# Kernel tuning notes

Measured on AMD Instinct MI355X. Metric: run time of the kernel, lower is better.

Reference implementation:

```python
import jax, jax.numpy as jnp
import numpy as np


def conv2d(x, w, b):
    # NCHW input, OIHW kernel, SAME padding, stride 1
    y = jax.lax.conv_general_dilated(x, w, (1, 1), 'SAME',
                                     dimension_numbers=('NCHW', 'OIHW', 'NCHW'))
    return y + b[None, :, None, None]


def maxpool2(x):
    return jax.lax.reduce_window(x, -jnp.inf, jax.lax.max,
                                 (1, 1, 2, 2), (1, 1, 2, 2), 'VALID')


def gelu(x):
    return jax.nn.gelu(x, approximate=False)  # torch default exact GELU


def up2(x):
    # nearest-neighbor upsample x2 (torch Upsample mode='nearest')
    return jnp.repeat(jnp.repeat(x, 2, axis=2), 2, axis=3)


DIM = 32
CODEBOOK_SIZE = 512
COMMIT_W = 1.0


def setup_inputs() -> dict:
    key = jax.random.key(0)
    ks = jax.random.split(key, 10)
    s = 0.1
    return {
        'x': jax.random.normal(ks[0], (32, 1, 256, 256), jnp.float32),
        'e1_w': jax.random.normal(ks[1], (16, 1, 3, 3), jnp.float32) * s,
        'e1_b': jnp.zeros((16,), jnp.float32),
        'e2_w': jax.random.normal(ks[2], (32, 16, 3, 3), jnp.float32) * s,
        'e2_b': jnp.zeros((32,), jnp.float32),
        'codebook': jax.random.normal(ks[3], (CODEBOOK_SIZE, DIM), jnp.float32),
        'd1_w': jax.random.normal(ks[4], (16, 32, 3, 3), jnp.float32) * s,
        'd1_b': jnp.zeros((16,), jnp.float32),
        'd2_w': jax.random.normal(ks[5], (1, 16, 3, 3), jnp.float32) * s,
        'd2_b': jnp.zeros((1,), jnp.float32),
    }


def reference(x, e1_w, e1_b, e2_w, e2_b, codebook, d1_w, d1_b, d2_w, d2_b):
    # ---- encoder ----
    h = conv2d(x, e1_w, e1_b)
    h = maxpool2(h)
    h = gelu(h)
    h = conv2d(h, e2_w, e2_b)
    h = maxpool2(h)                      # [B, 32, H/4, W/4]

    # ---- vector quantize (accept_image_fmap=True) ----
    B, C, H, W = h.shape
    flat = h.transpose(0, 2, 3, 1).reshape(-1, C)          # [N, C] tokens
    # squared euclidean distances to codebook
    d = ((flat * flat).sum(-1, keepdims=True)
         - 2.0 * flat @ codebook.T
         + (codebook * codebook).sum(-1))                   # [N, K]
    idx = jnp.argmin(d, axis=-1)                            # [N] int
    q = codebook[idx]                                       # gather [N, C]
    commit_loss = COMMIT_W * jnp.mean((jax.lax.stop_gradient(q) - flat) ** 2)
    # straight-through estimator
    q = flat + jax.lax.stop_gradient(q - flat)
    hq = q.reshape(B, H, W, C).transpose(0, 3, 1, 2)        # back to NCHW
    indices = idx.reshape(B, H, W)

    # ---- decoder ----
    y = up2(hq)
    y = conv2d(y, d1_w, d1_b)
    y = gelu(y)
    y = up2(y)
    y = conv2d(y, d2_w, d2_b)
    return jnp.clip(y, -1.0, 1.0), indices, commit_loss
```

## Files before the change

### kernel.cpp

```cpp
#include <hip/hip_runtime.h>
#include <math.h>

#define GELU(v) (0.5f * (v) * (1.0f + erff((v)*0.70710678118654752440f)))

typedef __attribute__((ext_vector_type(8))) short short8;
typedef __attribute__((ext_vector_type(4))) float f32x4;
typedef __attribute__((ext_vector_type(16))) float f32x16;
#define MFMA16 __builtin_amdgcn_mfma_f32_16x16x32_bf16
#define MFMA32 __builtin_amdgcn_mfma_f32_32x32x16_bf16

#define SPLIT3(V, U1, U2, U3)                                                  \
  unsigned U1 = __float_as_uint(V) & 0xFFFF0000u;                              \
  float _r1 = (V)-__uint_as_float(U1);                                         \
  unsigned U2 = __float_as_uint(_r1) & 0xFFFF0000u;                            \
  float _r2 = _r1 - __uint_as_float(U2);                                       \
  unsigned U3 = __float_as_uint(_r2) & 0xFFFF0000u;

__global__ __launch_bounds__(256) void k_fold(const float* __restrict__ e2w,
                                              const float* __restrict__ d1w,
                                              const float* __restrict__ d2w,
                                              const float* __restrict__ cb,
                                              float* __restrict__ fwd2,
                                              unsigned short* __restrict__ cbs,
                                              float* __restrict__ csqg,
                                              unsigned short* __restrict__ wfrag,
                                              unsigned short* __restrict__ wfd1) {
  int i = blockIdx.x * 256 + threadIdx.x;
  if (i < 256) {
    int j = i;
    int pt = j & 15, ic = j >> 4;
    int a = pt >> 3, b2 = (pt >> 2) & 1, dy = (pt >> 1) & 1, dx = pt & 1;
    const float* wsrc = d2w + ic * 9;
    float s = 0.f;
    for (int ky = 0; ky < 3; ++ky) {
      int rm = (a == 0) ? (ky == 0 ? 0 : 1) : (ky == 2 ? 1 : 0);
      if (rm != dy) continue;
      for (int kx = 0; kx < 3; ++kx) {
        int cm = (b2 == 0) ? (kx == 0 ? 0 : 1) : (kx == 2 ? 1 : 0);
        if (cm == dx) s += wsrc[ky * 3 + kx];
      }
    }
    fwd2[j] = s;
  } else if (i < 16640) {
    int j = i - 256;
    float v = cb[j];
    SPLIT3(v, u1, u2, u3)
    cbs[j] = (unsigned short)(u1 >> 16);
    cbs[16384 + j] = (unsigned short)(u2 >> 16);
    cbs[32768 + j] = (unsigned short)(u3 >> 16);
  } else if (i < 17152) {
    int c = i - 16640;
    const float* row = cb + (size_t)c * 32;
    float s = 0.f;
#pragma unroll
    for (int d = 0; d < 32; ++d) s = fmaf(row[d], row[d], s);
    csqg[c] = s;
  } else if (i < 30976) {
    int j = i - 17152;
    int p = j / 4608, rem = j - p * 4608;
    int t = rem >> 9, l2 = (rem >> 3) & 63, jj = rem & 7;
    float v = e2w[((l2 & 31) * 16 + ((l2 >> 5) * 8 + jj)) * 9 + t];
    SPLIT3(v, u1, u2, u3)
    unsigned short r = (p == 0)   ? (unsigned short)(u1 >> 16)
                       : (p == 1) ? (unsigned short)(u2 >> 16)
                                  : (unsigned short)(u3 >> 16);
    wfrag[j] = r;
  } else if (i < 86272) {
    int j = i - 30976;
    int slot = j >> 9, l2 = (j >> 3) & 63, jj = j & 7;
    int cx = slot / 36, rem = slot % 36;
    int r3 = rem / 12, rem2 = rem % 12;
    int kh = rem2 / 6, rem3 = rem2 % 6;
    int pp = rem3 / 3, part = rem3 % 3;
    int c = l2 & 31, hi = l2 >> 5;
    int oc = c & 15, b2 = c >> 4;
    int ic = kh * 16 + hi * 8 + jj;
    int dy = r3 - pp, dx = cx - b2;
    float s = 0.f;
    if ((unsigned)dy < 2u && (unsigned)dx < 2u) {
      const float* wsrc = d1w + (oc * 32 + ic) * 9;
      for (int ky = 0; ky < 3; ++ky) {
        int rm = (pp == 0) ? (ky == 0 ? 0 : 1) : (ky == 2 ? 1 : 0);
        if (rm != dy) continue;
        for (int kx = 0; kx < 3; ++kx) {
          int cm = (b2 == 0) ? (kx == 0 ? 0 : 1) : (kx == 2 ? 1 : 0);
          if (cm == dx) s += wsrc[ky * 3 + kx];
        }
      }
    }
    SPLIT3(s, u1, u2, u3)
    unsigned short r = (part == 0)   ? (unsigned short)(u1 >> 16)
                       : (part == 1) ? (unsigned short)(u2 >> 16)
                                     : (unsigned short)(u3 >> 16);
    wfd1[j] = r;
  }
}

__global__ __launch_bounds__(256) void k_enc1(const float* __restrict__ x,
                                              const float* __restrict__ w,
                                              const float* __restrict__ bias,
                                              float* __restrict__ h1) {
  int n = blockIdx.x;
  int ysl = n & 7, m = n >> 3;
  int b = m & 31, k = m >> 5;
  int yy = ysl * 16 + k * 2 + (threadIdx.x >> 7);
  int xx = threadIdx.x & 127;
  const float* xp = x + (size_t)b * 65536;
  int r0 = 2 * yy - 1, c0 = 2 * xx - 1;
  float in[4][4];
#pragma unroll
  for (int i = 0; i < 4; ++i) {
    int r = r0 + i;
    bool rv = (unsigned)r < 256u;
#pragma unroll
    for (int j = 0; j < 4; ++j) {
      int c = c0 + j;
      in[i][j] = (rv && (unsigned)c < 256u) ? xp[r * 256 + c] : 0.0f;
    }
  }
  float vout[16];
#pragma unroll
  for (int oc = 0; oc < 16; ++oc) {
    const float* wp = w + oc * 9;
    float s00 = 0.f, s01 = 0.f, s10 = 0.f, s11 = 0.f;
#pragma unroll
    for (int ky = 0; ky < 3; ++ky)
#pragma unroll
      for (int kx = 0; kx < 3; ++kx) {
        float wv = wp[ky * 3 + kx];
        s00 = fmaf(in[ky][kx], wv, s00);
        s01 = fmaf(in[ky][kx + 1], wv, s01);
        s10 = fmaf(in[ky + 1][kx], wv, s10);
        s11 = fmaf(in[ky + 1][kx + 1], wv, s11);
      }
    float mm = fmaxf(fmaxf(s00, s01), fmaxf(s10, s11)) + bias[oc];
    vout[oc] = GELU(mm);
  }
  float* op = h1 + (size_t)b * 262144 + ((size_t)yy * 128 + xx) * 16;
#pragma unroll
  for (int q = 0; q < 4; ++q) {
    float4 vq;
    vq.x = vout[4 * q + 0]; vq.y = vout[4 * q + 1];
    vq.z = vout[4 * q + 2]; vq.w = vout[4 * q + 3];
    *(float4*)(op + 4 * q) = vq;
  }
}

__global__ __launch_bounds__(256) void k_enc2(const float* __restrict__ h1,
                                              const unsigned short* __restrict__ wfrag,
                                              const float* __restrict__ bias,
                                              float* __restrict__ h2) {
  __shared__ __align__(16) unsigned short sA[3 * 2 * 10 * 34 * 8];
  const int PP = 2 * 10 * 34 * 8;
  int tid = threadIdx.x;
  int n = blockIdx.x;
  int xcd = n & 7, m = n >> 3;
  int ty = xcd * 2 + (m & 1);
  int q0 = m >> 1;
  int b = q0 >> 2, xt = q0 & 3;
  int X0 = xt * 32, Y0 = ty * 8;
  const float* ip = h1 + (size_t)b * 262144;
  for (int g = tid; g < 680; g += 256) {
    int pos = g >> 1, ich = g & 1;
    int yy = pos / 34, xx = pos - yy * 34;
    int y = Y0 - 1 + yy, xg = X0 - 1 + xx;
    float4 v0 = {0.f, 0.f, 0.f, 0.f}, v1 = {0.f, 0.f, 0.f, 0.f};
    if ((unsigned)y < 128u && (unsigned)xg < 128u) {
      const float* sp = ip + ((size_t)y * 128 + xg) * 16 + ich * 8;
      v0 = *(const float4*)(sp);
      v1 = *(const float4*)(sp + 4);
    }
    float vv[8] = {v0.x, v0.y, v0.z, v0.w, v1.x, v1.y, v1.z, v1.w};
    short8 p1, p2, p3;
#pragma unroll
    for (int e = 0; e < 8; ++e) {
      SPLIT3(vv[e], u1, u2, u3)
      p1[e] = (short)(u1 >> 16);
      p2[e] = (short)(u2 >> 16);
      p3[e] = (short)(u3 >> 16);
    }
    int si = ((ich * 10 + yy) * 34 + xx) * 8;
    *(short8*)(sA + si) = p1;
    *(short8*)(sA + PP + si) = p2;
    *(short8*)(sA + 2 * PP + si) = p3;
  }
  __syncthreads();

  int l = tid & 63, w = tid >> 6;
  int xl = l & 31, ich = l >> 5;
  f32x16 acc0[2], acc1[2];
#pragma unroll
  for (int s = 0; s < 2; ++s)
#pragma unroll
    for (int r = 0; r < 16; ++r) { acc0[s][r] = 0.f; acc1[s][r] = 0.f; }

#pragma unroll
  for (int t = 0; t < 9; ++t) {
    int dy = t / 3, dx = t % 3;
    int s = t & 1;
    const unsigned short* wb = wfrag + t * 512 + l * 8;
    short8 bf1 = *(const short8*)(wb);
    short8 bf2 = *(const short8*)(wb + 4608);
    short8 bf3 = *(const short8*)(wb + 9216);
    int g0 = ((ich * 10) + (2 * w + dy)) * 34 + xl + dx;
    const unsigned short* a0p = sA + g0 * 8;
    short8 a01 = *(const short8*)(a0p);
    short8 a02 = *(const short8*)(a0p + PP);
    short8 a03 = *(const short8*)(a0p + 2 * PP);
    const unsigned short* a1p = a0p + 34 * 8;
    short8 a11 = *(const short8*)(a1p);
    short8 a12 = *(const short8*)(a1p + PP);
    short8 a13 = *(const short8*)(a1p + 2 * PP);
    acc0[s] = MFMA32(a01, bf1, acc0[s], 0, 0, 0);
    acc0[s] = MFMA32(a01, bf2, acc0[s], 0, 0, 0);
    acc0[s] = MFMA32(a02, bf1, acc0[s], 0, 0, 0);
    acc0[s] = MFMA32(a02, bf2, acc0[s], 0, 0, 0);
    acc0[s] = MFMA32(a01, bf3, acc0[s], 0, 0, 0);
    acc0[s] = MFMA32(a03, bf1, acc0[s], 0, 0, 0);
    acc1[s] = MFMA32(a11, bf1, acc1[s], 0, 0, 0);
    acc1[s] = MFMA32(a11, bf2, acc1[s], 0, 0, 0);
    acc1[s] = MFMA32(a12, bf1, acc1[s], 0, 0, 0);
    acc1[s] = MFMA32(a12, bf2, acc1[s], 0, 0, 0);
    acc1[s] = MFMA32(a11, bf3, acc1[s], 0, 0, 0);
    acc1[s] = MFMA32(a13, bf1, acc1[s], 0, 0, 0);
  }

  float bv = bias[l & 31];
  int ypool = (Y0 >> 1) + w;
  float* op = h2 + (size_t)b * 131072 + (size_t)(l & 31) * 4096 + ypool * 64 + (X0 >> 1);
#pragma unroll
  for (int k = 0; k < 8; ++k) {
    float e0 = (acc0[0][2 * k] + acc0[1][2 * k]);
    float o0 = (acc0[0][2 * k + 1] + acc0[1][2 * k + 1]);
    float e1 = (acc1[0][2 * k] + acc1[1][2 * k]);
    float o1 = (acc1[0][2 * k + 1] + acc1[1][2 * k + 1]);
    float mm = fmaxf(fmaxf(e0, o0), fmaxf(e1, o1)) + bv;
    int row = ((2 * k) & 3) + 8 * ((2 * k) >> 2) + 4 * ich;
    op[row >> 1] = mm;
  }
}

__global__ __launch_bounds__(256) void k_vq(const float* __restrict__ h2,
                                            const unsigned short* __restrict__ cbs,
                                            const float* __restrict__ csqg,
                                            float* __restrict__ idxout,
                                            float* __restrict__ partial) {
  __shared__ __align__(16) unsigned short sA[3 * 256 * 40];
  __shared__ float sFsq[256];
  __shared__ float sBd[256];
  __shared__ int sBi[256];
  __shared__ float sred[4];
  int tid = threadIdx.x;
  int blk = blockIdx.x;
  int t0 = blk * 256;
  size_t abase = (size_t)(t0 >> 12) * 131072 + (t0 & 4095);

  {
    const float* src = h2 + abase + tid;
    float fsq = 0.f;
#pragma unroll
    for (int g = 0; g < 4; ++g) {
      short8 p1, p2, p3;
#pragma unroll
      for (int e = 0; e < 8; ++e) {
        float v = src[(g * 8 + e) * 4096];
        fsq = fmaf(v, v, fsq);
        SPLIT3(v, u1, u2, u3)
        p1[e] = (short)(u1 >> 16);
        p2[e] = (short)(u2 >> 16);
        p3[e] = (short)(u3 >> 16);
      }
      *(short8*)(sA + (0 * 256 + tid) * 40 + g * 8) = p1;
      *(short8*)(sA + (1 * 256 + tid) * 40 + g * 8) = p2;
      *(short8*)(sA + (2 * 256 + tid) * 40 + g * 8) = p3;
    }
    sFsq[tid] = fsq;
  }
  __syncthreads();

  int l = tid & 63, w = tid >> 6;
  int cl = l & 15, k0 = (l >> 4) * 8;
  short8 af[3][4];
#pragma unroll
  for (int p = 0; p < 3; ++p)
#pragma unroll
    for (int tq = 0; tq < 4; ++tq) {
      int tok = w * 64 + tq * 16 + cl;
      af[p][tq] = *(const short8*)(sA + (p * 256 + tok) * 40 + k0);
    }

  float bd[4][4];
  int bi[4][4];
#pragma unroll
  for (int a = 0; a < 4; ++a)
#pragma unroll
    for (int b = 0; b < 4; ++b) { bd[a][b] = 3.4e38f; bi[a][b] = 0; }

#define LOADB(S, CT)                                                           \
  {                                                                            \
    int col = (CT)*16 + cl;                                                    \
    b1##S = *(const short8*)(cbs + (0 * 512 + col) * 32 + k0);                 \
    b2##S = *(const short8*)(cbs + (1 * 512 + col) * 32 + k0);                 \
    b3##S = *(const short8*)(cbs + (2 * 512 + col) * 32 + k0);                 \
    cq##S = csqg[col];                                                         \
  }
#define COMPUTE(S, CT)                                                         \
  {                                                                            \
    _Pragma("unroll") for (int tq = 0; tq < 4; ++tq) {                         \
      f32x4 acc = {0.f, 0.f, 0.f, 0.f};                                        \
      acc = MFMA16(af[0][tq], b1##S, acc, 0, 0, 0);                            \
      acc = MFMA16(af[0][tq], b2##S, acc, 0, 0, 0);                            \
      acc = MFMA16(af[1][tq], b1##S, acc, 0, 0, 0);                            \
      acc = MFMA16(af[1][tq], b2##S, acc, 0, 0, 0);                            \
      acc = MFMA16(af[0][tq], b3##S, acc, 0, 0, 0);                            \
      acc = MFMA16(af[2][tq], b1##S, acc, 0, 0, 0);                            \
      _Pragma("unroll") for (int i = 0; i < 4; ++i) {                          \
        float d = fmaf(-2.f, acc[i], cq##S);                                   \
        if (d < bd[tq][i]) { bd[tq][i] = d; bi[tq][i] = (CT)*16 + cl; }        \
      }                                                                        \
    }                                                                          \
  }

  short8 b1A, b2A, b3A, b1B, b2B, b3B;
  float cqA, cqB;
  LOADB(A, 0)
  LOADB(B, 1)
#pragma unroll 1
  for (int ct = 0; ct < 32; ct += 2) {
    COMPUTE(A, ct)
    LOADB(A, (ct + 2) & 31)
    COMPUTE(B, ct + 1)
    LOADB(B, (ct + 3) & 31)
  }
#undef LOADB
#undef COMPUTE

#pragma unroll
  for (int tq = 0; tq < 4; ++tq)
#pragma unroll
    for (int i = 0; i < 4; ++i)
#pragma unroll
      for (int m = 1; m < 16; m <<= 1) {
        float od = __shfl_xor(bd[tq][i], m, 64);
        int ob = __shfl_xor(bi[tq][i], m, 64);
        if (od < bd[tq][i] || (od == bd[tq][i] && ob < bi[tq][i])) {
          bd[tq][i] = od;
          bi[tq][i] = ob;
        }
      }
  if (cl == 0) {
#pragma unroll
    for (int tq = 0; tq < 4; ++tq)
#pragma unroll
      for (int i = 0; i < 4; ++i) {
        int tokl = w * 64 + tq * 16 + (l >> 4) * 4 + i;
        sBi[tokl] = bi[tq][i];
        sBd[tokl] = bd[tq][i];
      }
  }
  __syncthreads();

  idxout[t0 + tid] = (float)sBi[tid];
  float loss = sBd[tid] + sFsq[tid];
#pragma unroll
  for (int off = 32; off > 0; off >>= 1) loss += __shfl_down(loss, off, 64);
  if (l == 0) sred[w] = loss;
  __syncthreads();
  if (tid == 0) partial[blk] = (sred[0] + sred[1]) + (sred[2] + sred[3]);
}

__global__ __launch_bounds__(256) void k_loss(const float* __restrict__ partial,
                                              float* __restrict__ lossout) {
  __shared__ float sred[4];
  int tid = threadIdx.x;
  float v = partial[tid] + partial[tid + 256];
#pragma unroll
  for (int off = 32; off > 0; off >>= 1) v += __shfl_down(v, off, 64);
  if ((tid & 63) == 0) sred[tid >> 6] = v;
  __syncthreads();
  if (tid == 0)
    lossout[0] = ((sred[0] + sred[1]) + (sred[2] + sred[3])) * (1.0f / 4194304.0f);
}

__global__ __launch_bounds__(256, 2) void k_dec1(const float* __restrict__ idxf,
                                                 const unsigned short* __restrict__ cbs,
                                                 const unsigned short* __restrict__ wfd1,
                                                 const float* __restrict__ bias,
                                                 float* __restrict__ o) {
  __shared__ __align__(16) unsigned short sA[3 * 12240];
  __shared__ int sIdx[340];
  const int PP = 12240;
  int tid = threadIdx.x;
  int b = blockIdx.y;
  int qx0 = (blockIdx.x & 1) * 32, qy0 = (blockIdx.x >> 1) * 8;
  const float* ib = idxf + (size_t)b * 4096;
  for (int i = tid; i < 340; i += 256) {
    int yy = i / 34, xx = i % 34;
    int y = qy0 - 1 + yy, x = qx0 - 1 + xx;
    sIdx[i] = ((unsigned)y < 64u && (unsigned)x < 64u) ? (int)ib[y * 64 + x] : -1;
  }
  __syncthreads();
  for (int i = tid; i < 4080; i += 256) {
    int pos = i / 12, sub = i % 12, part = sub >> 2, g = sub & 3;
    int idx = sIdx[pos];
    short8 v = {0, 0, 0, 0, 0, 0, 0, 0};
    if (idx >= 0) v = *(const short8*)(cbs + ((part << 9) + idx) * 32 + g * 8);
    *(short8*)(sA + part * PP + pos * 36 + g * 8) = v;
  }
  __syncthreads();

  int l = tid & 63, w = tid >> 6;
  int xl = l & 31, hi = l >> 5;
  f32x16 acc[2][2];
#pragma unroll
  for (int s = 0; s < 2; ++s)
#pragma unroll
    for (int p2 = 0; p2 < 2; ++p2)
#pragma unroll
      for (int r = 0; r < 16; ++r) acc[s][p2][r] = 0.f;

#pragma unroll
  for (int cx = 0; cx < 3; ++cx) {
    short8 Bf[4][2][3];
#pragma unroll
    for (int q = 0; q < 4; ++q) {
      int r3 = (q == 0) ? 0 : (q == 3) ? 2 : 1;
      int pq = (q >= 2) ? 1 : 0;
#pragma unroll
      for (int kh = 0; kh < 2; ++kh)
#pragma unroll
        for (int pt = 0; pt < 3; ++pt) {
          int slot = cx * 36 + r3 * 12 + kh * 6 + pq * 3 + pt;
          Bf[q][kh][pt] = *(const short8*)(wfd1 + (size_t)slot * 512 + l * 8);
        }
    }
#pragma unroll
    for (int ar = 0; ar < 4; ++ar) {
#pragma unroll
      for (int kh = 0; kh < 2; ++kh) {
        const unsigned short* ap =
            sA + ((2 * w + ar) * 34 + xl + cx) * 36 + kh * 16 + hi * 8;
        short8 a1 = *(const short8*)(ap);
        short8 a2 = *(const short8*)(ap + PP);
        short8 a3 = *(const short8*)(ap + 2 * PP);
#pragma unroll
        for (int s = 0; s < 2; ++s) {
          int ry = ar - s;
          if (ry < 0 || ry > 2) continue;
#pragma unroll
          for (int p2 = 0; p2 < 2; ++p2) {
            if ((ry == 0 && p2 == 1) || (ry == 2 && p2 == 0)) continue;
            int q = ry + p2;
            f32x16 t = acc[s][p2];
            t = MFMA32(a1, Bf[q][kh][0], t, 0, 0, 0);
            t = MFMA32(a1, Bf[q][kh][1], t, 0, 0, 0);
            t = MFMA32(a2, Bf[q][kh][0], t, 0, 0, 0);
            t = MFMA32(a2, Bf[q][kh][1], t, 0, 0, 0);
            t = MFMA32(a1, Bf[q][kh][2], t, 0, 0, 0);
            t = MFMA32(a3, Bf[q][kh][0], t, 0, 0, 0);
            acc[s][p2] = t;
          }
        }
      }
    }
  }

  float bv = bias[l & 15];
  int b2 = (l >> 4) & 1;
  float* ob = o + (size_t)b * 262144 + (size_t)(l & 15) * 16384 + (qx0 << 1) + b2;
#pragma unroll
  for (int s = 0; s < 2; ++s) {
    int qy = qy0 + 2 * w + s;
#pragma unroll
    for (int p2 = 0; p2 < 2; ++p2) {
      int Y = 2 * qy + p2;
      float* op = ob + Y * 128;
#pragma unroll
      for (int reg = 0; reg < 16; ++reg) {
        int rowval = (reg & 3) + 8 * (reg >> 2) + 4 * hi;
        op[2 * rowval] = GELU(acc[s][p2][reg] + bv);
      }
    }
  }
}

__global__ __launch_bounds__(256) void k_dec2(const float* __restrict__ d1,
                                              const float* __restrict__ fwd2,
                                              const float* __restrict__ bias,
                                              float* __restrict__ out) {
  __shared__ float st[16 * 360];
  int tid = threadIdx.x;
  int b = blockIdx.y;
  int R0 = (blockIdx.x >> 3) * 16, C0 = (blockIdx.x & 7) * 16;
  const float* ip = d1 + (size_t)b * 262144;
  for (int i = tid; i < 5184; i += 256) {
    int ic = i / 324, rr = (i % 324) / 18, cc = i % 18;
    int r = R0 - 1 + rr, c = C0 - 1 + cc;
    st[ic * 360 + rr * 20 + cc] =
        ((unsigned)r < 128u && (unsigned)c < 128u) ? ip[ic * 16384 + r * 128 + c] : 0.f;
  }
  __syncthreads();
  int lane = tid & 63, wid = tid >> 6;
  int qy = wid >> 1, qx = wid & 1;
  int ty = qy * 8 + (lane >> 3), tx = qx * 8 + (lane & 7);
  float acc[4] = {0.f, 0.f, 0.f, 0.f};
#pragma unroll 1
  for (int ic = 0; ic < 16; ++ic) {
    const float* t = st + ic * 360 + ty * 20 + tx;
    float i3[3][3];
#pragma unroll
    for (int dy = 0; dy < 3; ++dy)
#pragma unroll
      for (int dx = 0; dx < 3; ++dx) i3[dy][dx] = t[dy * 20 + dx];
    const float* wp = fwd2 + ic * 16;
#pragma unroll
    for (int p = 0; p < 4; ++p) {
      int a = p >> 1, b2 = p & 1;
#pragma unroll
      for (int tp = 0; tp < 4; ++tp) {
        int dy = tp >> 1, dx = tp & 1;
        acc[p] = fmaf(i3[a + dy][b2 + dx], wp[p * 4 + tp], acc[p]);
      }
    }
  }
  float bv = bias[0];
  int Y = 2 * (R0 + ty), X = 2 * (C0 + tx);
  float* op = out + (size_t)b * 65536 + Y * 256 + X;
  float2 r0v, r1v;
  r0v.x = fminf(1.0f, fmaxf(-1.0f, acc[0] + bv));
  r0v.y = fminf(1.0f, fmaxf(-1.0f, acc[1] + bv));
  r1v.x = fminf(1.0f, fmaxf(-1.0f, acc[2] + bv));
  r1v.y = fminf(1.0f, fmaxf(-1.0f, acc[3] + bv));
  *(float2*)op = r0v;
  *(float2*)(op + 256) = r1v;
}

extern "C" void kernel_launch(void* const* d_in, const int* in_sizes, int n_in,
                              void* d_out, int out_size, void* d_ws, size_t ws_size,
                              hipStream_t stream) {
  const float* x   = (const float*)d_in[0];
  const float* e1w = (const float*)d_in[1];
  const float* e1b = (const float*)d_in[2];
  const float* e2w = (const float*)d_in[3];
  const float* e2b = (const float*)d_in[4];
  const float* cb  = (const float*)d_in[5];
  const float* d1w = (const float*)d_in[6];
  const float* d1b = (const float*)d_in[7];
  const float* d2w = (const float*)d_in[8];
  const float* d2b = (const float*)d_in[9];

  float* out = (float*)d_out;
  float* y       = out;
  float* idxout  = out + 2097152;
  float* lossout = out + 2097152 + 131072;

  float* ws = (float*)d_ws;
  float* h1      = ws;
  float* h2      = ws + 8388608;
  float* partial = ws + 12582912;
  float* fwd2    = ws + 12596224;
  float* d1o     = h1;

  unsigned short* cbs = (unsigned short*)out;
  float* csqg = out + 24576;
  unsigned short* wfrag = (unsigned short*)(out + 25088);
  unsigned short* wfd1 = (unsigned short*)(out + 32000);

  k_fold<<<dim3(337), 256, 0, stream>>>(e2w, d1w, d2w, cb, fwd2, cbs, csqg, wfrag, wfd1);
  k_enc1<<<dim3(2048), 256, 0, stream>>>(x, e1w, e1b, h1);
  k_enc2<<<dim3(2048), 256, 0, stream>>>(h1, wfrag, e2b, h2);
  k_vq<<<dim3(512), 256, 0, stream>>>(h2, cbs, csqg, idxout, partial);
  k_loss<<<dim3(1), 256, 0, stream>>>(partial, lossout);
  k_dec1<<<dim3(16, 32), 256, 0, stream>>>(idxout, cbs, wfd1, d1b, d1o);
  k_dec2<<<dim3(64, 32), 256, 0, stream>>>(d1o, fwd2, d2b, y);
}
```

Measured before the change: 227.4 us.

## Switch dec1 output to channel-last and read codebook rows directly from global

The decoder's first conv no longer stages gathered codebook fragments in LDS. Each wave now handles one quantized row and loads A fragments straight from the global split codebook, and the grid doubles with half the rows per block. The intermediate d1 activation is written in NHWC (channel-innermost) layout, so dec2 can load 16 channels per pixel with float4 reads into a padded LDS tile and double-buffer its register windows across channels. This trades LDS staging and occupancy limits for more global/L2 gather traffic and strided scalar stores in dec1.

```diff
diff --git a/kernel.cpp b/kernel.cpp
--- a/kernel.cpp
+++ b/kernel.cpp
@@ -382,84 +382,70 @@
     lossout[0] = ((sred[0] + sred[1]) + (sred[2] + sred[3])) * (1.0f / 4194304.0f);
 }
 
-__global__ __launch_bounds__(256, 2) void k_dec1(const float* __restrict__ idxf,
-                                                 const unsigned short* __restrict__ cbs,
-                                                 const unsigned short* __restrict__ wfd1,
-                                                 const float* __restrict__ bias,
-                                                 float* __restrict__ o) {
-  __shared__ __align__(16) unsigned short sA[3 * 12240];
-  __shared__ int sIdx[340];
-  const int PP = 12240;
+__global__ __launch_bounds__(256) void k_dec1(const float* __restrict__ idxf,
+                                              const unsigned short* __restrict__ cbs,
+                                              const unsigned short* __restrict__ wfd1,
+                                              const float* __restrict__ bias,
+                                              float* __restrict__ o) {
+  __shared__ int sIdx[204];
   int tid = threadIdx.x;
   int b = blockIdx.y;
-  int qx0 = (blockIdx.x & 1) * 32, qy0 = (blockIdx.x >> 1) * 8;
+  int qx0 = (blockIdx.x & 1) * 32, qy0 = (blockIdx.x >> 1) * 4;
   const float* ib = idxf + (size_t)b * 4096;
-  for (int i = tid; i < 340; i += 256) {
-    int yy = i / 34, xx = i % 34;
+  if (tid < 204) {
+    int yy = tid / 34, xx = tid % 34;
     int y = qy0 - 1 + yy, x = qx0 - 1 + xx;
-    sIdx[i] = ((unsigned)y < 64u && (unsigned)x < 64u) ? (int)ib[y * 64 + x] : -1;
-  }
-  __syncthreads();
-  for (int i = tid; i < 4080; i += 256) {
-    int pos = i / 12, sub = i % 12, part = sub >> 2, g = sub & 3;
-    int idx = sIdx[pos];
-    short8 v = {0, 0, 0, 0, 0, 0, 0, 0};
-    if (idx >= 0) v = *(const short8*)(cbs + ((part << 9) + idx) * 32 + g * 8);
-    *(short8*)(sA + part * PP + pos * 36 + g * 8) = v;
+    sIdx[tid] = ((unsigned)y < 64u && (unsigned)x < 64u) ? (int)ib[y * 64 + x] : -1;
   }
   __syncthreads();
 
   int l = tid & 63, w = tid >> 6;
   int xl = l & 31, hi = l >> 5;
-  f32x16 acc[2][2];
-#pragma unroll
-  for (int s = 0; s < 2; ++s)
-#pragma unroll
-    for (int p2 = 0; p2 < 2; ++p2)
-#pragma unroll
-      for (int r = 0; r < 16; ++r) acc[s][p2][r] = 0.f;
+  f32x16 acc[2];
+#pragma unroll
+  for (int p2 = 0; p2 < 2; ++p2)
+#pragma unroll
+    for (int r = 0; r < 16; ++r) acc[p2][r] = 0.f;
 
 #pragma unroll
   for (int cx = 0; cx < 3; ++cx) {
-    short8 Bf[4][2][3];
-#pragma unroll
-    for (int q = 0; q < 4; ++q) {
-      int r3 = (q == 0) ? 0 : (q == 3) ? 2 : 1;
-      int pq = (q >= 2) ? 1 : 0;
-#pragma unroll
-      for (int kh = 0; kh < 2; ++kh)
+#pragma unroll
+    for (int kh = 0; kh < 2; ++kh) {
+      short8 Bf[4][3];
+#pragma unroll
+      for (int q = 0; q < 4; ++q) {
+        int r3 = (q == 0) ? 0 : (q == 3) ? 2 : 1;
+        int pq = (q >= 2) ? 1 : 0;
 #pragma unroll
         for (int pt = 0; pt < 3; ++pt) {
           int slot = cx * 36 + r3 * 12 + kh * 6 + pq * 3 + pt;
-          Bf[q][kh][pt] = *(const short8*)(wfd1 + (size_t)slot * 512 + l * 8);
-        }
-    }
-#pragma unroll
-    for (int ar = 0; ar < 4; ++ar) {
-#pragma unroll
-      for (int kh = 0; kh < 2; ++kh) {
-        const unsigned short* ap =
-            sA + ((2 * w + ar) * 34 + xl + cx) * 36 + kh * 16 + hi * 8;
-        short8 a1 = *(const short8*)(ap);
-        short8 a2 = *(const short8*)(ap + PP);
-        short8 a3 = *(const short8*)(ap + 2 * PP);
-#pragma unroll
-        for (int s = 0; s < 2; ++s) {
-          int ry = ar - s;
-          if (ry < 0 || ry > 2) continue;
-#pragma unroll
-          for (int p2 = 0; p2 < 2; ++p2) {
-            if ((ry == 0 && p2 == 1) || (ry == 2 && p2 == 0)) continue;
-            int q = ry + p2;
-            f32x16 t = acc[s][p2];
-            t = MFMA32(a1, Bf[q][kh][0], t, 0, 0, 0);
-            t = MFMA32(a1, Bf[q][kh][1], t, 0, 0, 0);
-            t = MFMA32(a2, Bf[q][kh][0], t, 0, 0, 0);
-            t = MFMA32(a2, Bf[q][kh][1], t, 0, 0, 0);
-            t = MFMA32(a1, Bf[q][kh][2], t, 0, 0, 0);
-            t = MFMA32(a3, Bf[q][kh][0], t, 0, 0, 0);
-            acc[s][p2] = t;
-          }
+          Bf[q][pt] = *(const short8*)(wfd1 + (size_t)slot * 512 + l * 8);
+        }
+      }
+#pragma unroll
+      for (int ry = 0; ry < 3; ++ry) {
+        int idx = sIdx[(w + ry) * 34 + xl + cx];
+        short8 a1 = {0, 0, 0, 0, 0, 0, 0, 0};
+        short8 a2 = {0, 0, 0, 0, 0, 0, 0, 0};
+        short8 a3 = {0, 0, 0, 0, 0, 0, 0, 0};
+        if (idx >= 0) {
+          const unsigned short* ap = cbs + (size_t)idx * 32 + kh * 16 + hi * 8;
+          a1 = *(const short8*)(ap);
+          a2 = *(const short8*)(ap + 16384);
+          a3 = *(const short8*)(ap + 32768);
+        }
+#pragma unroll
+        for (int p2 = 0; p2 < 2; ++p2) {
+          if ((ry == 0 && p2 == 1) || (ry == 2 && p2 == 0)) continue;
+          int q = ry + p2;
+          f32x16 t = acc[p2];
+          t = MFMA32(a1, Bf[q][0], t, 0, 0, 0);
+          t = MFMA32(a1, Bf[q][1], t, 0, 0, 0);
+          t = MFMA32(a2, Bf[q][0], t, 0, 0, 0);
+          t = MFMA32(a2, Bf[q][1], t, 0, 0, 0);
+          t = MFMA32(a1, Bf[q][2], t, 0, 0, 0);
+          t = MFMA32(a3, Bf[q][0], t, 0, 0, 0);
+          acc[p2] = t;
         }
       }
     }
@@ -467,59 +453,80 @@
 
   float bv = bias[l & 15];
   int b2 = (l >> 4) & 1;
-  float* ob = o + (size_t)b * 262144 + (size_t)(l & 15) * 16384 + (qx0 << 1) + b2;
-#pragma unroll
-  for (int s = 0; s < 2; ++s) {
-    int qy = qy0 + 2 * w + s;
-#pragma unroll
-    for (int p2 = 0; p2 < 2; ++p2) {
-      int Y = 2 * qy + p2;
-      float* op = ob + Y * 128;
-#pragma unroll
-      for (int reg = 0; reg < 16; ++reg) {
-        int rowval = (reg & 3) + 8 * (reg >> 2) + 4 * hi;
-        op[2 * rowval] = GELU(acc[s][p2][reg] + bv);
-      }
-    }
-  }
-}
-
+  int oc = l & 15;
+  int qy = qy0 + w;
+  float* ob = o + (size_t)b * 262144;
+#pragma unroll
+  for (int p2 = 0; p2 < 2; ++p2) {
+    int Y = 2 * qy + p2;
+#pragma unroll
+    for (int reg = 0; reg < 16; ++reg) {
+      int rowval = (reg & 3) + 8 * (reg >> 2) + 4 * hi;
+      int X = qx0 * 2 + 2 * rowval + b2;
+      ob[((size_t)Y * 128 + X) * 16 + oc] = GELU(acc[p2][reg] + bv);
+    }
+  }
+}
+
+__device__ __forceinline__ void d2_loadi3(float (&dst)[3][3], const float* t) {
+#pragma unroll
+  for (int dy = 0; dy < 3; ++dy)
+#pragma unroll
+    for (int dx = 0; dx < 3; ++dx) dst[dy][dx] = t[(dy * 18 + dx) * 17];
+}
 __global__ __launch_bounds__(256) void k_dec2(const float* __restrict__ d1,
                                               const float* __restrict__ fwd2,
                                               const float* __restrict__ bias,
                                               float* __restrict__ out) {
-  __shared__ float st[16 * 360];
+  __shared__ float st[18 * 18 * 17];
   int tid = threadIdx.x;
   int b = blockIdx.y;
   int R0 = (blockIdx.x >> 3) * 16, C0 = (blockIdx.x & 7) * 16;
   const float* ip = d1 + (size_t)b * 262144;
-  for (int i = tid; i < 5184; i += 256) {
-    int ic = i / 324, rr = (i % 324) / 18, cc = i % 18;
+  for (int i = tid; i < 1296; i += 256) {
+    int pos = i >> 2, q = i & 3;
+    int rr = pos / 18, cc = pos % 18;
     int r = R0 - 1 + rr, c = C0 - 1 + cc;
-    st[ic * 360 + rr * 20 + cc] =
-        ((unsigned)r < 128u && (unsigned)c < 128u) ? ip[ic * 16384 + r * 128 + c] : 0.f;
+    float4 v = {0.f, 0.f, 0.f, 0.f};
+    if ((unsigned)r < 128u && (unsigned)c < 128u)
+      v = *(const float4*)(ip + ((size_t)r * 128 + c) * 16 + q * 4);
+    float* dp = st + (rr * 18 + cc) * 17 + q * 4;
+    dp[0] = v.x; dp[1] = v.y; dp[2] = v.z; dp[3] = v.w;
   }
   __syncthreads();
   int lane = tid & 63, wid = tid >> 6;
   int qy = wid >> 1, qx = wid & 1;
   int ty = qy * 8 + (lane >> 3), tx = qx * 8 + (lane & 7);
   float acc[4] = {0.f, 0.f, 0.f, 0.f};
+  const float* tb = st + (ty * 18 + tx) * 17;
+  float i3A[3][3], i3B[3][3];
+  d2_loadi3(i3A, tb);
 #pragma unroll 1
-  for (int ic = 0; ic < 16; ++ic) {
-    const float* t = st + ic * 360 + ty * 20 + tx;
-    float i3[3][3];
-#pragma unroll
-    for (int dy = 0; dy < 3; ++dy)
-#pragma unroll
-      for (int dx = 0; dx < 3; ++dx) i3[dy][dx] = t[dy * 20 + dx];
-    const float* wp = fwd2 + ic * 16;
-#pragma unroll
-    for (int p = 0; p < 4; ++p) {
-      int a = p >> 1, b2 = p & 1;
-#pragma unroll
-      for (int tp = 0; tp < 4; ++tp) {
-        int dy = tp >> 1, dx = tp & 1;
-        acc[p] = fmaf(i3[a + dy][b2 + dx], wp[p * 4 + tp], acc[p]);
+  for (int ic = 0; ic < 16; ic += 2) {
+    d2_loadi3(i3B, tb + (ic + 1));
+    {
+      const float* wp = fwd2 + ic * 16;
+#pragma unroll
+      for (int p = 0; p < 4; ++p) {
+        int a = p >> 1, b2 = p & 1;
+#pragma unroll
+        for (int tp = 0; tp < 4; ++tp) {
+          int dy = tp >> 1, dx = tp & 1;
+          acc[p] = fmaf(i3A[a + dy][b2 + dx], wp[p * 4 + tp], acc[p]);
+        }
+      }
+    }
+    d2_loadi3(i3A, tb + ((ic + 2) & 15));
+    {
+      const float* wp = fwd2 + (ic + 1) * 16;
+#pragma unroll
+      for (int p = 0; p < 4; ++p) {
+        int a = p >> 1, b2 = p & 1;
+#pragma unroll
+        for (int tp = 0; tp < 4; ++tp) {
+          int dy = tp >> 1, dx = tp & 1;
+          acc[p] = fmaf(i3B[a + dy][b2 + dx], wp[p * 4 + tp], acc[p]);
+        }
       }
     }
   }
@@ -571,6 +578,6 @@
   k_enc2<<<dim3(2048), 256, 0, stream>>>(h1, wfrag, e2b, h2);
   k_vq<<<dim3(512), 256, 0, stream>>>(h2, cbs, csqg, idxout, partial);
   k_loss<<<dim3(1), 256, 0, stream>>>(partial, lossout);
-  k_dec1<<<dim3(16, 32), 256, 0, stream>>>(idxout, cbs, wfd1, d1b, d1o);
+  k_dec1<<<dim3(32, 32), 256, 0, stream>>>(idxout, cbs, wfd1, d1b, d1o);
   k_dec2<<<dim3(64, 32), 256, 0, stream>>>(d1o, fwd2, d2b, y);
 }
```

Result: faster. 210.7 us (-7.3%).
